# Kernel tuning notes

Measured on AMD Instinct MI355X. Metric: run time of the kernel, lower is better.

Reference implementation:

```python
import jax, jax.numpy as jnp
import numpy as np

EPS = 1e-12  # torch F.normalize default eps


def setup_inputs() -> dict:
    key = jax.random.key(0)
    ks = jax.random.split(key, 7)
    dim, heads = 128, 8
    b, c, s, h, w = 2, dim, 3, 128, 128
    sc = 1.0 / np.sqrt(dim)
    return {
        "x": jax.random.normal(ks[0], (b, c, s, h, w), dtype=jnp.float32),
        "Wq": jax.random.normal(ks[1], (dim, dim), dtype=jnp.float32) * sc,
        "Wk": jax.random.normal(ks[2], (dim, dim), dtype=jnp.float32) * sc,
        "Wv": jax.random.normal(ks[3], (dim, dim), dtype=jnp.float32) * sc,
        "Wp": jax.random.normal(ks[4], (dim, dim), dtype=jnp.float32) * sc,
        "bp": jax.random.normal(ks[5], (dim,), dtype=jnp.float32) * 0.01,
        "rescale": jnp.ones((heads, 1, 1), dtype=jnp.float32),
    }


def _l2norm(t):
    # torch F.normalize(p=2, dim=-1): t / max(||t||, eps)
    n = jnp.sqrt(jnp.sum(t * t, axis=-1, keepdims=True))
    return t / jnp.maximum(n, EPS)


def reference(x, Wq, Wk, Wv, Wp, bp, rescale):
    b, c, s, h, w = x.shape
    heads = rescale.shape[0]
    d = c // heads
    n = h * w * s
    # [b,c,s,h,w] -> [b,h,w,s,c] -> [b, n, c]
    xt = jnp.transpose(x, (0, 3, 4, 2, 1)).reshape(b, n, c)
    # torch Linear: y = x @ W.T
    q = xt @ Wq.T
    k = xt @ Wk.T
    v = xt @ Wv.T
    # [b,n,heads,d] -> [b,heads,d,n] (channel attention: tokens along last axis)
    def to_heads(t):
        return jnp.transpose(t.reshape(b, n, heads, d), (0, 2, 3, 1))
    q, k, v = to_heads(q), to_heads(k), to_heads(v)
    q = _l2norm(q)
    k = _l2norm(k)
    # attn: [b,heads,d,d] = k @ q^T over token axis n
    attn = jnp.einsum('bhdn,bhen->bhde', k, q)
    attn = attn * rescale  # rescale broadcasts as [heads,1,1]
    attn = jax.nn.softmax(attn, axis=-1)
    out = jnp.einsum('bhde,bhen->bhdn', attn, v)  # [b,heads,d,n]
    # [b,heads,d,n] -> [b,n,heads*d]
    out = jnp.transpose(out, (0, 3, 1, 2)).reshape(b, n, c)
    out = out @ Wp.T + bp
    # [b,n,c] -> [b,h,w,s,c] -> [b,h,w,c,s] -> [b,c,s,h,w]
    out = out.reshape(b, h, w, s, c)
    out = jnp.transpose(out, (0, 1, 2, 4, 3))
    out = jnp.transpose(out, (0, 3, 4, 1, 2))
    return out
```

## Files before the change

kernel.cpp:

```cpp
#include <hip/hip_runtime.h>
#include <hip/hip_bf16.h>

typedef __bf16 bf16_t;
typedef __bf16 bf16x4 __attribute__((ext_vector_type(4)));
typedef __bf16 bf16x8 __attribute__((ext_vector_type(8)));
typedef float f32x4 __attribute__((ext_vector_type(4)));

#define NTOK 49152
#define CDIM 128
#define CHUNKS 128
#define KT 384
#define STEPS 12

__device__ inline f32x4 mfma16(bf16x8 a, bf16x8 b, f32x4 c) {
  return __builtin_amdgcn_mfma_f32_16x16x32_bf16(a, b, c, 0, 0, 0);
}

#define BARRIER() do { asm volatile("s_waitcnt lgkmcnt(0)" ::: "memory"); \
    __builtin_amdgcn_s_barrier(); } while (0)

#define STAGE_LOAD(st, step)                               \
  {                                                        \
    const float* p_ = gsrc + (step) * 32;                  \
    st[0] = *(const f32x4*)(p_ + 0);                       \
    st[1] = *(const f32x4*)(p_ + 4);                       \
    st[2] = *(const f32x4*)(p_ + 8);                       \
    st[3] = *(const f32x4*)(p_ + 12);                      \
  }
#define CVT4(v) (bf16x4){(bf16_t)(v)[0], (bf16_t)(v)[1], (bf16_t)(v)[2], (bf16_t)(v)[3]}
#define STAGE_WRITE(st, buf)                               \
  {                                                        \
    bf16_t* t_ = &tile[buf][0];                            \
    *(bf16x4*)&t_[cg0 * 8 + 0] = CVT4(st[0]);              \
    *(bf16x4*)&t_[cg0 * 8 + 4] = CVT4(st[1]);              \
    *(bf16x4*)&t_[cg1 * 8 + 0] = CVT4(st[2]);              \
    *(bf16x4*)&t_[cg1 * 8 + 4] = CVT4(st[3]);              \
  }
#define MFMA_PHASE(buf)                                                     \
  {                                                                         \
    bf16x8 frag[8];                                                         \
    _Pragma("unroll")                                                       \
    for (int g = 0; g < 8; ++g)                                             \
      frag[g] = *(const bf16x8*)&tile[buf][(g * 64 + lane) * 8];            \
    bf16x8 a0, a1;                                                          \
    if (wave == 0)      { a0 = frag[0]; a1 = frag[1]; }                     \
    else if (wave == 1) { a0 = frag[2]; a1 = frag[3]; }                     \
    else if (wave == 2) { a0 = frag[4]; a1 = frag[5]; }                     \
    else                { a0 = frag[6]; a1 = frag[7]; }                     \
    _Pragma("unroll")                                                       \
    for (int j = 0; j < 8; ++j) {                                           \
      acc[0][j] = mfma16(a0, frag[j], acc[0][j]);                           \
      acc[1][j] = mfma16(a1, frag[j], acc[1][j]);                           \
    }                                                                       \
  }

__global__ __launch_bounds__(256) void k1_gram(const float* __restrict__ x,
                                               float* __restrict__ part) {
  const int blk = blockIdx.x;
  const int b = blk >> 7, chunk = blk & 127;
  const float* Xb = x + (size_t)b * CDIM * NTOK;
  const int tid = threadIdx.x, wave = tid >> 6, lane = tid & 63;

  __shared__ __align__(16) bf16_t tile[2][128 * 32];

  const int sch = tid >> 1, shalf = tid & 1;
  const float* gsrc = Xb + (size_t)sch * NTOK + chunk * KT + shalf * 16;
  const int c16base = ((sch >> 4) << 6) + (sch & 15);
  const int cg0 = c16base + ((shalf * 2) << 4);
  const int cg1 = c16base + ((shalf * 2 + 1) << 4);

  f32x4 stA[4], stB[4];
  f32x4 acc[2][8];
#pragma unroll
  for (int t = 0; t < 2; ++t)
#pragma unroll
    for (int j = 0; j < 8; ++j) acc[t][j] = (f32x4){0.f, 0.f, 0.f, 0.f};

  STAGE_LOAD(stA, 0);
  STAGE_WRITE(stA, 0);
  STAGE_LOAD(stB, 1);
  BARRIER();

  for (int kk = 0; kk < STEPS; kk += 2) {
    if (kk + 2 < STEPS) STAGE_LOAD(stA, kk + 2);
    STAGE_WRITE(stB, 1);
    MFMA_PHASE(0);
    BARRIER();
    if (kk + 3 < STEPS) STAGE_LOAD(stB, kk + 3);
    if (kk + 2 < STEPS) STAGE_WRITE(stA, 0);
    MFMA_PHASE(1);
    BARRIER();
  }

  float* pb = part + ((size_t)(b * CHUNKS + chunk) << 14);
#pragma unroll
  for (int t = 0; t < 2; ++t)
#pragma unroll
    for (int j = 0; j < 8; ++j)
      *(f32x4*)&pb[((((t * 8 + j) << 8) + tid) << 2)] = acc[t][j];
}

__global__ __launch_bounds__(256) void k2s(const float* __restrict__ part,
                                           float* __restrict__ S) {
  const int gid = blockIdx.x * 256 + threadIdx.x;
  const int e = gid & 16383, b = gid >> 14;
  const float* p = part + ((size_t)b << 21) + e;
  float a0 = 0.f, a1 = 0.f, a2 = 0.f, a3 = 0.f;
#pragma unroll 8
  for (int i = 0; i < 128; i += 4) {
    a0 += p[(size_t)(i + 0) << 14];
    a1 += p[(size_t)(i + 1) << 14];
    a2 += p[(size_t)(i + 2) << 14];
    a3 += p[(size_t)(i + 3) << 14];
  }
  const float s = (a0 + a1) + (a2 + a3);
  const int g4 = e >> 2, rg = e & 3;
  const int tj = g4 >> 8, t = tj >> 3, j = tj & 7;
  const int t2 = g4 & 255, w2 = t2 >> 6, q2 = (t2 >> 4) & 3, r2 = t2 & 15;
  const int row = w2 * 32 + t * 16 + q2 * 4 + rg, col = j * 16 + r2;
  S[((size_t)b << 14) + row * 128 + col] = s;
}

__global__ __launch_bounds__(256) void kattn(const float* __restrict__ S,
                                             const float* __restrict__ Wk,
                                             const float* __restrict__ Wq,
                                             const float* __restrict__ resc,
                                             float* __restrict__ attn) {
  const int blk = blockIdx.x;
  const int b = blk >> 3, h = blk & 7;
  const int tid = threadIdx.x;

  __shared__ float S_l[128][132];
  __shared__ float Wk_l[16][128], Wq_l[16][128];
  __shared__ float Tk_l[16][132], Tq_l[16][132];
  __shared__ float dK[16], dQ[16];

  {
    const float* Sb = S + ((size_t)b << 14);
#pragma unroll
    for (int q = 0; q < 16; ++q) {
      const int idx = q * 256 + tid;
      const int row = idx >> 5, c4 = (idx & 31) << 2;
      *(f32x4*)&S_l[row][c4] = *(const f32x4*)(Sb + row * 128 + c4);
    }
#pragma unroll
    for (int k = 0; k < 8; ++k) {
      const int idx = k * 256 + tid;
      Wk_l[idx >> 7][idx & 127] = Wk[h * 2048 + idx];
      Wq_l[idx >> 7][idx & 127] = Wq[h * 2048 + idx];
    }
  }
  __syncthreads();

  {
    const int d2 = tid >> 5;
    const int j0 = (tid & 31) * 4;
    f32x4 aK0 = (f32x4){0.f,0.f,0.f,0.f}, aK1 = (f32x4){0.f,0.f,0.f,0.f};
    f32x4 aQ0 = (f32x4){0.f,0.f,0.f,0.f}, aQ1 = (f32x4){0.f,0.f,0.f,0.f};
#pragma unroll 1
    for (int cb = 0; cb < 4; ++cb) {
      f32x4 wk0[8], wk1[8], wq0[8], wq1[8];
#pragma unroll
      for (int q = 0; q < 8; ++q) {
        wk0[q] = *(const f32x4*)&Wk_l[d2][cb * 32 + q * 4];
        wk1[q] = *(const f32x4*)&Wk_l[d2 + 8][cb * 32 + q * 4];
        wq0[q] = *(const f32x4*)&Wq_l[d2][cb * 32 + q * 4];
        wq1[q] = *(const f32x4*)&Wq_l[d2 + 8][cb * 32 + q * 4];
      }
#pragma unroll
      for (int q = 0; q < 8; ++q) {
#pragma unroll
        for (int cc = 0; cc < 4; ++cc) {
          const int c = cb * 32 + q * 4 + cc;
          const f32x4 sv = *(const f32x4*)&S_l[c][j0];
          aK0 += sv * wk0[q][cc];
          aK1 += sv * wk1[q][cc];
          aQ0 += sv * wq0[q][cc];
          aQ1 += sv * wq1[q][cc];
        }
      }
    }
    *(f32x4*)&Tk_l[d2][j0]     = aK0;
    *(f32x4*)&Tk_l[d2 + 8][j0] = aK1;
    *(f32x4*)&Tq_l[d2][j0]     = aQ0;
    *(f32x4*)&Tq_l[d2 + 8][j0] = aQ1;
  }
  __syncthreads();

  {
    const int d = tid >> 4, e = tid & 15;
    f32x4 gacc = (f32x4){0.f,0.f,0.f,0.f};
    f32x4 kacc = (f32x4){0.f,0.f,0.f,0.f};
    f32x4 qacc = (f32x4){0.f,0.f,0.f,0.f};
#pragma unroll
    for (int j4 = 0; j4 < 32; ++j4) {
      const f32x4 tk = *(const f32x4*)&Tk_l[d][j4 * 4];
      const f32x4 wq = *(const f32x4*)&Wq_l[e][j4 * 4];
      gacc += tk * wq;
      if (e == 0) kacc += tk * (*(const f32x4*)&Wk_l[d][j4 * 4]);
      if (d == 0) qacc += (*(const f32x4*)&Tq_l[e][j4 * 4]) * wq;
    }
    if (e == 0) dK[d] = kacc[0] + kacc[1] + kacc[2] + kacc[3];
    if (d == 0) dQ[e] = qacc[0] + qacc[1] + qacc[2] + qacc[3];
    __syncthreads();
    const float g = gacc[0] + gacc[1] + gacc[2] + gacc[3];
    const float nk = fmaxf(sqrtf(fmaxf(dK[d], 0.f)), 1e-12f);
    const float nq = fmaxf(sqrtf(fmaxf(dQ[e], 0.f)), 1e-12f);
    float pre = g / (nk * nq) * resc[h];
    float mx = pre;
#pragma unroll
    for (int m = 1; m < 16; m <<= 1) mx = fmaxf(mx, __shfl_xor(mx, m, 64));
    const float p = expf(pre - mx);
    float sum = p;
#pragma unroll
    for (int m = 1; m < 16; m <<= 1) sum += __shfl_xor(sum, m, 64);
    attn[blk * 256 + tid] = p / sum;
  }
}

__global__ __launch_bounds__(256) void k3_p(const float* __restrict__ attn,
                                            const float* __restrict__ Wp,
                                            const float* __restrict__ Wv,
                                            bf16_t* __restrict__ Phi) {
  const int blk = blockIdx.x;
  const int b = blk >> 7, rrow = blk & 127;
  const int tid = threadIdx.x;
  __shared__ float M[128];
  if (tid < 128) {
    const int h = tid >> 4, e = tid & 15;
    const float* A = attn + (size_t)(b * 8 + h) * 256;
    const float* wp = Wp + rrow * 128 + h * 16;
    float m = 0.f;
#pragma unroll
    for (int d = 0; d < 16; ++d) m += wp[d] * A[d * 16 + e];
    M[tid] = m;
  }
  __syncthreads();
  if (tid < 128) {
    const int c = tid;
    float p = 0.f;
#pragma unroll 4
    for (int j = 0; j < 128; ++j) p += M[j] * Wv[j * 128 + c];
    Phi[((size_t)b << 14) + rrow * 128 + c] = (bf16_t)p;
  }
}

__global__ __launch_bounds__(256) void k4_out(const float* __restrict__ x,
                                              const bf16_t* __restrict__ Phi,
                                              const float* __restrict__ bp,
                                              float* __restrict__ out) {
  const int blk = blockIdx.x;
  const int b = blk / 768, tg = blk % 768;
  const float* Xb = x + (size_t)b * CDIM * NTOK;
  const bf16_t* Ph = Phi + ((size_t)b << 14);
  float* Ob = out + (size_t)b * CDIM * NTOK;
  const int tid = threadIdx.x, wave = tid >> 6, lane = tid & 63;
  const int r = lane & 15, quad = lane >> 4;
  const int tok0 = tg * 64;

  __shared__ __align__(16) char smem[64 * 68 * 4];
  bf16_t* tile = (bf16_t*)smem;
  float* tbuf = (float*)smem;

  {
    const int sch = tid >> 1, shalf = tid & 1;
    const float* p = Xb + (size_t)sch * NTOK + tok0 + shalf * 32;
    f32x4 st[8];
#pragma unroll
    for (int q = 0; q < 8; ++q) st[q] = *(const f32x4*)(p + q * 4);
    const int chunk_hi = ((sch >> 5) << 8) + (((sch >> 3) & 3) << 4);
    const int ei = sch & 7;
#pragma unroll
    for (int j = 0; j < 32; ++j) {
      const int tok = shalf * 32 + j;
      const int chunk = chunk_hi + ((tok >> 4) << 6) + (tok & 15);
      tile[chunk * 8 + ei] = (bf16_t)st[j >> 2][j & 3];
    }
  }
  __syncthreads();

  f32x4 acc[8];
#pragma unroll
  for (int m = 0; m < 8; ++m) acc[m] = (f32x4){0.f, 0.f, 0.f, 0.f};

#pragma unroll
  for (int step = 0; step < 4; ++step) {
    const bf16x8 bfr = *(const bf16x8*)&tile[(step * 256 + wave * 64 + lane) * 8];
#pragma unroll
    for (int m = 0; m < 8; ++m) {
      const bf16x8 ah = *(const bf16x8*)(Ph + (16 * m + r) * 128 + step * 32 + quad * 8);
      acc[m] = mfma16(ah, bfr, acc[m]);
    }
  }

  __syncthreads();
#pragma unroll
  for (int half = 0; half < 2; ++half) {
#pragma unroll
    for (int mm = 0; mm < 4; ++mm) {
#pragma unroll
      for (int reg = 0; reg < 4; ++reg)
        tbuf[(mm * 16 + quad * 4 + reg) * 68 + wave * 16 + r] = acc[half * 4 + mm][reg];
    }
    __syncthreads();
#pragma unroll
    for (int rep = 0; rep < 4; ++rep) {
      const int idx = rep * 256 + tid, rloc = idx >> 4, g = idx & 15;
      f32x4 v = *(const f32x4*)&tbuf[rloc * 68 + g * 4];
      const int row = half * 64 + rloc;
      const float bb = bp[row];
      v[0] += bb; v[1] += bb; v[2] += bb; v[3] += bb;
      *(f32x4*)&Ob[(size_t)row * NTOK + tok0 + g * 4] = v;
    }
    if (half == 0) __syncthreads();
  }
}

extern "C" void kernel_launch(void* const* d_in, const int* in_sizes, int n_in,
                              void* d_out, int out_size, void* d_ws, size_t ws_size,
                              hipStream_t stream) {
  const float* x    = (const float*)d_in[0];
  const float* Wq   = (const float*)d_in[1];
  const float* Wk   = (const float*)d_in[2];
  const float* Wv   = (const float*)d_in[3];
  const float* Wp   = (const float*)d_in[4];
  const float* bp   = (const float*)d_in[5];
  const float* resc = (const float*)d_in[6];
  float* out = (float*)d_out;

  char* ws = (char*)d_ws;
  float*  S    = (float*)(ws + 0);
  float*  attn = (float*)(ws + 131072);
  bf16_t* Phi  = (bf16_t*)(ws + 147456);
  float* part  = (float*)d_out;

  k1_gram<<<2 * CHUNKS, 256, 0, stream>>>(x, part);
  k2s<<<128, 256, 0, stream>>>(part, S);
  kattn<<<16, 256, 0, stream>>>(S, Wk, Wq, resc, attn);
  k3_p<<<256, 256, 0, stream>>>(attn, Wp, Wv, Phi);
  k4_out<<<1536, 256, 0, stream>>>(x, Phi, bp, out);
}
```

Measured before the change: 178.6 us.

## Split partial-Gram reduction into two vectorized stages and prefetch earlier

After: 174.3 us. 2.4% less time.

```diff
diff --git a/kernel.cpp b/kernel.cpp
--- a/kernel.cpp
+++ b/kernel.cpp
@@ -84,9 +84,9 @@
   for (int kk = 0; kk < STEPS; kk += 2) {
     if (kk + 2 < STEPS) STAGE_LOAD(stA, kk + 2);
     STAGE_WRITE(stB, 1);
+    if (kk + 3 < STEPS) STAGE_LOAD(stB, kk + 3);
     MFMA_PHASE(0);
     BARRIER();
-    if (kk + 3 < STEPS) STAGE_LOAD(stB, kk + 3);
     if (kk + 2 < STEPS) STAGE_WRITE(stA, 0);
     MFMA_PHASE(1);
     BARRIER();
@@ -100,25 +100,31 @@
       *(f32x4*)&pb[((((t * 8 + j) << 8) + tid) << 2)] = acc[t][j];
 }
 
-__global__ __launch_bounds__(256) void k2s(const float* __restrict__ part,
-                                           float* __restrict__ S) {
+__global__ __launch_bounds__(256) void k2a_reduce(const float* __restrict__ part,
+                                                  float* __restrict__ part2) {
   const int gid = blockIdx.x * 256 + threadIdx.x;
-  const int e = gid & 16383, b = gid >> 14;
-  const float* p = part + ((size_t)b << 21) + e;
-  float a0 = 0.f, a1 = 0.f, a2 = 0.f, a3 = 0.f;
+  const int e4 = gid & 4095, sl = (gid >> 12) & 7, b = gid >> 15;
+  const float* p = part + ((size_t)(b * CHUNKS + sl * 16) << 14) + e4 * 4;
+  f32x4 s = (f32x4){0.f, 0.f, 0.f, 0.f};
 #pragma unroll 8
-  for (int i = 0; i < 128; i += 4) {
-    a0 += p[(size_t)(i + 0) << 14];
-    a1 += p[(size_t)(i + 1) << 14];
-    a2 += p[(size_t)(i + 2) << 14];
-    a3 += p[(size_t)(i + 3) << 14];
-  }
-  const float s = (a0 + a1) + (a2 + a3);
-  const int g4 = e >> 2, rg = e & 3;
+  for (int i = 0; i < 16; ++i) s += *(const f32x4*)(p + ((size_t)i << 14));
+  *(f32x4*)(part2 + ((size_t)(b * 8 + sl) << 14) + e4 * 4) = s;
+}
+
+__global__ __launch_bounds__(256) void k2b_reduce(const float* __restrict__ part2,
+                                                  float* __restrict__ S) {
+  const int gid = blockIdx.x * 256 + threadIdx.x;
+  const int g4 = gid & 4095, b = gid >> 12;
+  f32x4 s = (f32x4){0.f, 0.f, 0.f, 0.f};
+#pragma unroll
+  for (int sl = 0; sl < 8; ++sl)
+    s += *(const f32x4*)(part2 + ((size_t)(b * 8 + sl) << 14) + g4 * 4);
   const int tj = g4 >> 8, t = tj >> 3, j = tj & 7;
-  const int t2 = g4 & 255, w2 = t2 >> 6, q2 = (t2 >> 4) & 3, r2 = t2 & 15;
-  const int row = w2 * 32 + t * 16 + q2 * 4 + rg, col = j * 16 + r2;
-  S[((size_t)b << 14) + row * 128 + col] = s;
+  const int tid2 = g4 & 255, wave = tid2 >> 6, quad = (tid2 >> 4) & 3, r = tid2 & 15;
+  const int row0 = wave * 32 + t * 16 + quad * 4, col = j * 16 + r;
+  float* Sb = S + ((size_t)b << 14);
+#pragma unroll
+  for (int reg = 0; reg < 4; ++reg) Sb[(row0 + reg) * 128 + col] = s[reg];
 }
 
 __global__ __launch_bounds__(256) void kattn(const float* __restrict__ S,
@@ -333,9 +339,11 @@
   float*  attn = (float*)(ws + 131072);
   bf16_t* Phi  = (bf16_t*)(ws + 147456);
   float* part  = (float*)d_out;
+  float* part2 = (float*)((char*)d_out + 16777216);
 
   k1_gram<<<2 * CHUNKS, 256, 0, stream>>>(x, part);
-  k2s<<<128, 256, 0, stream>>>(part, S);
+  k2a_reduce<<<256, 256, 0, stream>>>(part, part2);
+  k2b_reduce<<<32, 256, 0, stream>>>(part2, S);
   kattn<<<16, 256, 0, stream>>>(S, Wk, Wq, resc, attn);
   k3_p<<<256, 256, 0, stream>>>(attn, Wp, Wv, Phi);
   k4_out<<<1536, 256, 0, stream>>>(x, Phi, bp, out);
```
